# Performance work log

Hardware: AMD Instinct MI355X
Metric: run time of the kernel (lower is better)

## Reference

```python
import jax, jax.numpy as jnp
import numpy as np

HIDDEN = 512
H2 = HIDDEN * 2  # 1024
SEQ = 65536


def setup_inputs() -> dict:
    key = jax.random.key(0)
    k0, k1, k2, k3 = jax.random.split(key, 4)
    outputs = jax.random.normal(k0, (SEQ, H2), dtype=jnp.float32)
    # nn.Linear(2H, 2H): weight [out, in], bias [out]
    lim = 1.0 / np.sqrt(H2)
    W = jax.random.uniform(k1, (H2, H2), dtype=jnp.float32, minval=-lim, maxval=lim)
    b = jax.random.uniform(k2, (H2,), dtype=jnp.float32, minval=-lim, maxval=lim)
    weight_vec = jax.random.normal(k3, (1, H2), dtype=jnp.float32)
    return {"outputs": outputs, "W": W, "b": b, "weight_vec": weight_vec}


def reference(outputs, W, b, weight_vec):
    # energy_i = dot(weight_vec, W @ outputs[i] + b)  -> batched:
    energy = jnp.einsum("sh,oh->so", outputs, W) + b          # [S, 2H]
    attn_energies = energy @ weight_vec.reshape(-1)            # [S]
    attn = jax.nn.softmax(attn_energies, axis=0)               # [S]
    return attn[None, None, :]                                 # [1, 1, S]
```

## Files before the change

kernel.cpp:

```cpp
#include <hip/hip_runtime.h>
#include <math.h>

#define SEQ 65536
#define H2  1024

__global__ void reduce_W_partial(const float* __restrict__ W,
                                 const float* __restrict__ wv,
                                 float* __restrict__ partial) {
    const int h  = blockIdx.x * 256 + threadIdx.x;
    const int oc = blockIdx.y;
    const int o0 = oc * 16;
    float acc = 0.0f;
#pragma unroll
    for (int j = 0; j < 16; ++j)
        acc += wv[o0 + j] * W[(size_t)(o0 + j) * H2 + h];
    partial[oc * H2 + h] = acc;
}

__global__ void fold_v(const float* __restrict__ partial,
                       float* __restrict__ v) {
    const int h = blockIdx.x * 256 + threadIdx.x;
    float acc = 0.0f;
#pragma unroll 8
    for (int oc = 0; oc < 64; ++oc) acc += partial[oc * H2 + h];
    v[h] = acc;
}

__global__ void __launch_bounds__(256) row_dot(
        const float4* __restrict__ outputs,
        const float4* __restrict__ v4,
        float* __restrict__ e,
        float* __restrict__ bmax,
        float* __restrict__ bsum) {
    const int b    = blockIdx.x;
    const int t    = threadIdx.x;
    const int w    = t >> 6;
    const int lane = t & 63;

    const float4 vr0 = v4[lane];
    const float4 vr1 = v4[lane + 64];
    const float4 vr2 = v4[lane + 128];
    const float4 vr3 = v4[lane + 192];

    const int r0 = b * 64 + w * 16;
    float m = -INFINITY, s = 0.0f, myval = 0.0f;

#pragma unroll 4
    for (int j = 0; j < 16; ++j) {
        const float4* rp = outputs + (size_t)(r0 + j) * 256;
        const float4 a0 = rp[lane];
        const float4 a1 = rp[lane + 64];
        const float4 a2 = rp[lane + 128];
        const float4 a3 = rp[lane + 192];
        float acc = a0.x * vr0.x + a0.y * vr0.y + a0.z * vr0.z + a0.w * vr0.w;
        acc      += a1.x * vr1.x + a1.y * vr1.y + a1.z * vr1.z + a1.w * vr1.w;
        acc      += a2.x * vr2.x + a2.y * vr2.y + a2.z * vr2.z + a2.w * vr2.w;
        acc      += a3.x * vr3.x + a3.y * vr3.y + a3.z * vr3.z + a3.w * vr3.w;
#pragma unroll
        for (int off = 1; off < 64; off <<= 1)
            acc += __shfl_xor(acc, off, 64);
        if (lane == j) myval = acc;
        const float d = acc - m;
        if (d > 0.0f) { s = s * __expf(-d) + 1.0f; m = acc; }
        else          { s += __expf(d); }
    }
    if (lane < 16) e[r0 + lane] = myval;

    __shared__ float lm[4], ls[4];
    if (lane == 0) { lm[w] = m; ls[w] = s; }
    __syncthreads();
    if (t == 0) {
        float M = lm[0], S = ls[0];
#pragma unroll
        for (int i = 1; i < 4; ++i) {
            const float Mn = fmaxf(M, lm[i]);
            S = S * __expf(M - Mn) + ls[i] * __expf(lm[i] - Mn);
            M = Mn;
        }
        bmax[b] = M;
        bsum[b] = S;
    }
}

__global__ void __launch_bounds__(256) softmax_norm_fused(
        const float* __restrict__ e,
        const float* __restrict__ bmax,
        const float* __restrict__ bsum,
        float* __restrict__ out) {
    const int t = threadIdx.x;
    float M = -INFINITY, S = 0.0f;
#pragma unroll
    for (int i = 0; i < 4; ++i) {
        const int idx = t + 256 * i;
        const float m2 = bmax[idx], s2 = bsum[idx];
        const float Mn = fmaxf(M, m2);
        S = S * __expf(M - Mn) + s2 * __expf(m2 - Mn);
        M = Mn;
    }
    __shared__ float rm[256], rs[256];
    rm[t] = M; rs[t] = S;
    __syncthreads();
    for (int stride = 128; stride > 0; stride >>= 1) {
        if (t < stride) {
            const float M1 = rm[t], S1 = rs[t];
            const float M2 = rm[t + stride], S2 = rs[t + stride];
            const float Mn = fmaxf(M1, M2);
            rm[t] = Mn;
            rs[t] = S1 * __expf(M1 - Mn) + S2 * __expf(M2 - Mn);
        }
        __syncthreads();
    }
    const float Mg  = rm[0];
    const float inv = 1.0f / rs[0];

    const int i = blockIdx.x * 256 + t;
    out[i] = __expf(e[i] - Mg) * inv;
}

extern "C" void kernel_launch(void* const* d_in, const int* in_sizes, int n_in,
                              void* d_out, int out_size, void* d_ws, size_t ws_size,
                              hipStream_t stream) {
    const float* outputs = (const float*)d_in[0];
    const float* W       = (const float*)d_in[1];
    const float* wv      = (const float*)d_in[3];
    float* out = (float*)d_out;

    float* ws = (float*)d_ws;
    float* v       = ws;
    float* partial = ws + H2;
    float* e       = partial + 64 * H2;
    float* bmax    = e + SEQ;
    float* bsum    = bmax + 1024;

    reduce_W_partial<<<dim3(4, 64), 256, 0, stream>>>(W, wv, partial);
    fold_v<<<4, 256, 0, stream>>>(partial, v);
    row_dot<<<1024, 256, 0, stream>>>((const float4*)outputs,
                                      (const float4*)v, e, bmax, bsum);
    softmax_norm_fused<<<SEQ / 256, 256, 0, stream>>>(e, bmax, bsum, out);
}
```

Baseline: 376.4 us.

## Fuse row dot and softmax normalization via cooperative grid sync

Merges the row-dot kernel and the softmax normalization kernel into one cooperative kernel that performs a grid-wide sync after publishing per-block max/sum. Each block then reduces the global stats and writes its own normalized outputs from registers, removing the energy buffer round-trip and a kernel launch. It also switches the main input reads to nontemporal loads. The cost is a grid barrier, and the launch requires all 1024 blocks to be co-resident.

```diff
diff --git a/kernel.cpp b/kernel.cpp
--- a/kernel.cpp
+++ b/kernel.cpp
@@ -1,8 +1,13 @@
 #include <hip/hip_runtime.h>
+#include <hip/hip_cooperative_groups.h>
 #include <math.h>
+
+namespace cg = cooperative_groups;
 
 #define SEQ 65536
 #define H2  1024
+
+typedef float f4 __attribute__((ext_vector_type(4)));
 
 __global__ void reduce_W_partial(const float* __restrict__ W,
                                  const float* __restrict__ wv,
@@ -26,32 +31,32 @@
     v[h] = acc;
 }
 
-__global__ void __launch_bounds__(256) row_dot(
-        const float4* __restrict__ outputs,
-        const float4* __restrict__ v4,
-        float* __restrict__ e,
+__global__ void __launch_bounds__(256, 4) row_softmax(
+        const f4* __restrict__ outputs,
+        const f4* __restrict__ v4,
         float* __restrict__ bmax,
-        float* __restrict__ bsum) {
+        float* __restrict__ bsum,
+        float* __restrict__ out) {
     const int b    = blockIdx.x;
     const int t    = threadIdx.x;
     const int w    = t >> 6;
     const int lane = t & 63;
 
-    const float4 vr0 = v4[lane];
-    const float4 vr1 = v4[lane + 64];
-    const float4 vr2 = v4[lane + 128];
-    const float4 vr3 = v4[lane + 192];
+    const f4 vr0 = v4[lane];
+    const f4 vr1 = v4[lane + 64];
+    const f4 vr2 = v4[lane + 128];
+    const f4 vr3 = v4[lane + 192];
 
     const int r0 = b * 64 + w * 16;
     float m = -INFINITY, s = 0.0f, myval = 0.0f;
 
 #pragma unroll 4
     for (int j = 0; j < 16; ++j) {
-        const float4* rp = outputs + (size_t)(r0 + j) * 256;
-        const float4 a0 = rp[lane];
-        const float4 a1 = rp[lane + 64];
-        const float4 a2 = rp[lane + 128];
-        const float4 a3 = rp[lane + 192];
+        const f4* rp = outputs + (size_t)(r0 + j) * 256;
+        const f4 a0 = __builtin_nontemporal_load(rp + lane);
+        const f4 a1 = __builtin_nontemporal_load(rp + lane + 64);
+        const f4 a2 = __builtin_nontemporal_load(rp + lane + 128);
+        const f4 a3 = __builtin_nontemporal_load(rp + lane + 192);
         float acc = a0.x * vr0.x + a0.y * vr0.y + a0.z * vr0.z + a0.w * vr0.w;
         acc      += a1.x * vr1.x + a1.y * vr1.y + a1.z * vr1.z + a1.w * vr1.w;
         acc      += a2.x * vr2.x + a2.y * vr2.y + a2.z * vr2.z + a2.w * vr2.w;
@@ -64,9 +69,9 @@
         if (d > 0.0f) { s = s * __expf(-d) + 1.0f; m = acc; }
         else          { s += __expf(d); }
     }
-    if (lane < 16) e[r0 + lane] = myval;
 
     __shared__ float lm[4], ls[4];
+    __shared__ float rm[256], rs[256];
     if (lane == 0) { lm[w] = m; ls[w] = s; }
     __syncthreads();
     if (t == 0) {
@@ -80,14 +85,9 @@
         bmax[b] = M;
         bsum[b] = S;
     }
-}
 
-__global__ void __launch_bounds__(256) softmax_norm_fused(
-        const float* __restrict__ e,
-        const float* __restrict__ bmax,
-        const float* __restrict__ bsum,
-        float* __restrict__ out) {
-    const int t = threadIdx.x;
+    cg::this_grid().sync();
+
     float M = -INFINITY, S = 0.0f;
 #pragma unroll
     for (int i = 0; i < 4; ++i) {
@@ -97,7 +97,6 @@
         S = S * __expf(M - Mn) + s2 * __expf(m2 - Mn);
         M = Mn;
     }
-    __shared__ float rm[256], rs[256];
     rm[t] = M; rs[t] = S;
     __syncthreads();
     for (int stride = 128; stride > 0; stride >>= 1) {
@@ -113,8 +112,7 @@
     const float Mg  = rm[0];
     const float inv = 1.0f / rs[0];
 
-    const int i = blockIdx.x * 256 + t;
-    out[i] = __expf(e[i] - Mg) * inv;
+    if (lane < 16) out[r0 + lane] = __expf(myval - Mg) * inv;
 }
 
 extern "C" void kernel_launch(void* const* d_in, const int* in_sizes, int n_in,
@@ -128,13 +126,15 @@
     float* ws = (float*)d_ws;
     float* v       = ws;
     float* partial = ws + H2;
-    float* e       = partial + 64 * H2;
-    float* bmax    = e + SEQ;
+    float* bmax    = partial + 64 * H2;
     float* bsum    = bmax + 1024;
 
     reduce_W_partial<<<dim3(4, 64), 256, 0, stream>>>(W, wv, partial);
     fold_v<<<4, 256, 0, stream>>>(partial, v);
-    row_dot<<<1024, 256, 0, stream>>>((const float4*)outputs,
-                                      (const float4*)v, e, bmax, bsum);
-    softmax_norm_fused<<<SEQ / 256, 256, 0, stream>>>(e, bmax, bsum, out);
+
+    const f4* o4  = (const f4*)outputs;
+    const f4* v4p = (const f4*)v;
+    void* args[] = {(void*)&o4, (void*)&v4p, (void*)&bmax, (void*)&bsum, (void*)&out};
+    hipLaunchCooperativeKernel((const void*)row_softmax, dim3(1024), dim3(256),
+                               args, 0, stream);
 }
```

Measured after the change: 461.9 us. 22.7% more time.
